# Performance work log

Hardware: AMD Instinct MI355X
Metric: run time of the kernel (lower is better)

Reference implementation:

```python
import jax, jax.numpy as jnp
import numpy as np

B, S, D = 8, 2048, 512

def setup_inputs() -> dict:
    key = jax.random.key(0)
    k1, k2 = jax.random.split(key)
    lstm_out = jax.random.normal(k1, (B, S, D), dtype=jnp.float32)
    # xavier_uniform init for [D, D]
    limit = float(np.sqrt(6.0 / (D + D)))
    attention_weights = jax.random.uniform(k2, (D, D), dtype=jnp.float32, minval=-limit, maxval=limit)
    return {"lstm_out": lstm_out, "attention_weights": attention_weights}

def reference(lstm_out, attention_weights):
    # scores[b,i,j] = tanh( (x W) x^T )
    proj = jnp.einsum('bsd,de->bse', lstm_out, attention_weights)          # [B,S,D]
    scores = jnp.tanh(jnp.einsum('bsd,btd->bst', proj, lstm_out))          # [B,S,S]
    attn = jax.nn.softmax(scores, axis=-1)                                 # [B,S,S]
    return jnp.einsum('bst,btd->bsd', attn, lstm_out)                      # [B,S,D]
```

## Files before the change

### kernel.cpp

```cpp
#include <hip/hip_runtime.h>
#include <hip/hip_bf16.h>

typedef __bf16 bf16;
typedef __attribute__((ext_vector_type(8))) __bf16 bf16x8;
typedef __attribute__((ext_vector_type(4))) float floatx4;

#define NPART 16
#define NSLOT 32

__device__ __forceinline__ void gl_lds16(const bf16* g, bf16* l) {
    __builtin_amdgcn_global_load_lds(
        (const __attribute__((address_space(1))) unsigned int*)g,
        (__attribute__((address_space(3))) unsigned int*)l,
        16, 0, 0);
}

__device__ __forceinline__ void swizzle_mn(int& bm, int& bn) {
    int gx = gridDim.x;
    int f  = blockIdx.y * gx + blockIdx.x;
    int st = f >> 3, r = f & 7;
    int mgroups = gx >> 2;
    bm = (st % mgroups) * 4 + (r & 3);
    bn = (st / mgroups) * 2 + (r >> 2);
}

__global__ __launch_bounds__(256) void cast_both(const float* __restrict__ in,
                                                 bf16* __restrict__ outn,
                                                 bf16* __restrict__ outt,
                                                 int R, int C) {
    __shared__ float tile[32][33];
    const long long bz = blockIdx.z;
    in   += bz * (long long)R * C;
    outn += bz * (long long)R * C;
    outt += bz * (long long)R * C;
    const int r0 = blockIdx.x * 32, c0 = blockIdx.y * 32;
    const int tx = threadIdx.x & 31, ty = threadIdx.x >> 5;
#pragma unroll
    for (int i = 0; i < 32; i += 8) {
        float v = in[(long long)(r0 + ty + i) * C + (c0 + tx)];
        tile[ty + i][tx] = v;
        outn[(long long)(r0 + ty + i) * C + (c0 + tx)] = (bf16)v;
    }
    __syncthreads();
#pragma unroll
    for (int i = 0; i < 32; i += 8)
        outt[(long long)(c0 + ty + i) * R + (r0 + tx)] = (bf16)tile[tx][ty + i];
}

__global__ __launch_bounds__(256) void cast_transpose(const float* __restrict__ in,
                                                      bf16* __restrict__ out,
                                                      int R, int C) {
    __shared__ float tile[32][33];
    const int r0 = blockIdx.x * 32, c0 = blockIdx.y * 32;
    const int tx = threadIdx.x & 31, ty = threadIdx.x >> 5;
#pragma unroll
    for (int i = 0; i < 32; i += 8)
        tile[ty + i][tx] = in[(long long)(r0 + ty + i) * C + (c0 + tx)];
    __syncthreads();
#pragma unroll
    for (int i = 0; i < 32; i += 8)
        out[(long long)(c0 + ty + i) * R + (r0 + tx)] = (bf16)tile[tx][ty + i];
}

__device__ __forceinline__ float fast_tanh(float v) {
    float e = __expf(2.0f * v);
    return 1.0f - 2.0f / (e + 1.0f);
}

template <int MODE>
__global__ __launch_bounds__(256) void gemm128(const bf16* __restrict__ A,
                                               const bf16* __restrict__ Bm,
                                               void* __restrict__ Cout,
                                               float* __restrict__ rpart,
                                               int M, int N, int K,
                                               long long batchA, long long batchB,
                                               long long batchC, long long batchR) {
    const long long bz = blockIdx.z;
    A  += bz * batchA;
    Bm += bz * batchB;

    __shared__ bf16 As[2][128 * 64];
    __shared__ bf16 Bs[2][128 * 64];
    __shared__ float rs[128];

    const int t    = threadIdx.x;
    const int lane = t & 63;
    const int wave = t >> 6;
    const int quad = lane >> 4;
    const int l16  = lane & 15;

    int bm, bn;
    swizzle_mn(bm, bn);
    const int m0 = bm * 128;
    const int n0 = bn * 128;
    const int wm = (wave >> 1) * 64;
    const int wn = (wave & 1) * 64;

    floatx4 acc[4][4] = {};

    const int ra = t >> 3;
    const int ca = (((t & 7) ^ (ra & 7))) * 8;
    const long long rstep = 32LL * K;
    const bf16* Abase = A + (long long)(m0 + ra) * K + ca;
    const bf16* Bbase = Bm + (long long)(n0 + ra) * K + ca;

    const int cq0 = ((quad) ^ (l16 & 7)) * 8;
    const int cq1 = ((4 + quad) ^ (l16 & 7)) * 8;

    if (MODE == 2) {
        if (t < 128) {
            const float* pp = rpart + (bz * batchR + m0 + t) * NSLOT;
            float s = 0.f;
#pragma unroll
            for (int c = 0; c < NSLOT / 4; ++c) {
                float4 p = ((const float4*)pp)[c];
                s += (p.x + p.y) + (p.z + p.w);
            }
            rs[t] = 1.0f / s;
        }
    }

    auto stage = [&](int buf, int k0) {
#pragma unroll
        for (int i = 0; i < 4; ++i) {
            gl_lds16(Abase + k0 + i * rstep, &As[buf][(t + 256 * i) * 8]);
            gl_lds16(Bbase + k0 + i * rstep, &Bs[buf][(t + 256 * i) * 8]);
        }
    };

    auto compute = [&](int buf) {
#pragma unroll
        for (int s = 0; s < 2; ++s) {
            const int cq = s ? cq1 : cq0;
            bf16x8 af[4], bfr[4];
#pragma unroll
            for (int i = 0; i < 4; ++i)
                af[i] = *(const bf16x8*)(&As[buf][(wm + i * 16 + l16) * 64 + cq]);
#pragma unroll
            for (int j = 0; j < 4; ++j)
                bfr[j] = *(const bf16x8*)(&Bs[buf][(wn + j * 16 + l16) * 64 + cq]);
#pragma unroll
            for (int i = 0; i < 4; ++i)
#pragma unroll
                for (int j = 0; j < 4; ++j)
                    acc[i][j] = __builtin_amdgcn_mfma_f32_16x16x32_bf16(af[i], bfr[j], acc[i][j], 0, 0, 0);
        }
    };

    stage(0, 0);
    __syncthreads();

    for (int k0 = 0; k0 < K; k0 += 128) {
        if (k0 + 64 < K) stage(1, k0 + 64);
        compute(0);
        __syncthreads();
        if (k0 + 128 < K) stage(0, k0 + 128);
        compute(1);
        __syncthreads();
    }

    if (MODE == 1) {
        bf16* Cg = (bf16*)Cout + bz * batchC;
        const int slot = bn * 2 + (wave & 1);
#pragma unroll
        for (int i = 0; i < 4; ++i)
#pragma unroll
            for (int r = 0; r < 4; ++r) {
                long long row = m0 + wm + i * 16 + quad * 4 + r;
                float s = 0.f;
#pragma unroll
                for (int j = 0; j < 4; ++j) {
                    float v = __expf(fast_tanh(acc[i][j][r]));
                    s += v;
                    Cg[row * (long long)N + (n0 + wn + j * 16 + l16)] = (bf16)v;
                }
#pragma unroll
                for (int msk = 1; msk < 16; msk <<= 1) s += __shfl_xor(s, msk);
                if (l16 == 0)
                    rpart[(bz * batchR + row) * NSLOT + slot] = s;
            }
    } else {
        float* Og = (float*)Cout + bz * batchC;
#pragma unroll
        for (int i = 0; i < 4; ++i)
#pragma unroll
            for (int r = 0; r < 4; ++r) {
                int rl = wm + i * 16 + quad * 4 + r;
                float inv = rs[rl];
                long long row = m0 + rl;
#pragma unroll
                for (int j = 0; j < 4; ++j)
                    Og[row * (long long)N + (n0 + wn + j * 16 + l16)] = acc[i][j][r] * inv;
            }
    }
}

__global__ __launch_bounds__(256) void gemm64_nt(const bf16* __restrict__ A,
                                                 const bf16* __restrict__ Bm,
                                                 bf16* __restrict__ Cout,
                                                 int M, int N, int K) {
    __shared__ bf16 As[2][64 * 64];
    __shared__ bf16 Bs[2][128 * 64];

    const int t    = threadIdx.x;
    const int lane = t & 63;
    const int wave = t >> 6;
    const int quad = lane >> 4;
    const int l16  = lane & 15;

    const int m0 = blockIdx.x * 64;
    const int n0 = blockIdx.y * 128;
    const int wn = wave * 32;

    floatx4 acc[4][2] = {};

    const int ra = t >> 3;
    const int ca = (((t & 7) ^ (ra & 7))) * 8;
    const long long rstep = 32LL * K;
    const bf16* Abase = A + (long long)(m0 + ra) * K + ca;
    const bf16* Bbase = Bm + (long long)(n0 + ra) * K + ca;

    const int cq0 = ((quad) ^ (l16 & 7)) * 8;
    const int cq1 = ((4 + quad) ^ (l16 & 7)) * 8;

    auto stage = [&](int buf, int k0) {
#pragma unroll
        for (int i = 0; i < 2; ++i)
            gl_lds16(Abase + k0 + i * rstep, &As[buf][(t + 256 * i) * 8]);
#pragma unroll
        for (int i = 0; i < 4; ++i)
            gl_lds16(Bbase + k0 + i * rstep, &Bs[buf][(t + 256 * i) * 8]);
    };

    auto compute = [&](int buf) {
#pragma unroll
        for (int s = 0; s < 2; ++s) {
            const int cq = s ? cq1 : cq0;
            bf16x8 af[4], bfr[2];
#pragma unroll
            for (int i = 0; i < 4; ++i)
                af[i] = *(const bf16x8*)(&As[buf][(i * 16 + l16) * 64 + cq]);
#pragma unroll
            for (int j = 0; j < 2; ++j)
                bfr[j] = *(const bf16x8*)(&Bs[buf][(wn + j * 16 + l16) * 64 + cq]);
#pragma unroll
            for (int i = 0; i < 4; ++i)
#pragma unroll
                for (int j = 0; j < 2; ++j)
                    acc[i][j] = __builtin_amdgcn_mfma_f32_16x16x32_bf16(af[i], bfr[j], acc[i][j], 0, 0, 0);
        }
    };

    stage(0, 0);
    __syncthreads();

    for (int k0 = 0; k0 < K; k0 += 128) {
        if (k0 + 64 < K) stage(1, k0 + 64);
        compute(0);
        __syncthreads();
        if (k0 + 128 < K) stage(0, k0 + 128);
        compute(1);
        __syncthreads();
    }

#pragma unroll
    for (int i = 0; i < 4; ++i)
#pragma unroll
        for (int r = 0; r < 4; ++r) {
            long long row = m0 + i * 16 + quad * 4 + r;
#pragma unroll
            for (int j = 0; j < 2; ++j)
                Cout[row * (long long)N + (n0 + wn + j * 16 + l16)] = (bf16)acc[i][j][r];
        }
}

extern "C" void kernel_launch(void* const* d_in, const int* in_sizes, int n_in,
                              void* d_out, int out_size, void* d_ws, size_t ws_size,
                              hipStream_t stream) {
    const int B = 8, S = 2048, D = 512;
    const float* x = (const float*)d_in[0];
    const float* W = (const float*)d_in[1];
    float* out = (float*)d_out;

    const size_t nx = (size_t)B * S * D;
    const size_t nw = (size_t)D * D;

    char* ws = (char*)d_ws;
    auto al = [](size_t v) { return (v + 255) & ~(size_t)255; };
    size_t off = 0;
    bf16* xb = (bf16*)(ws + off); off = al(off + nx * 2);
    bf16* xt = (bf16*)(ws + off); off = al(off + nx * 2);
    bf16* pb = (bf16*)(ws + off); off = al(off + nx * 2);
    bf16* wt = (bf16*)(ws + off); off = al(off + nw * 2);
    float* rpart = (float*)(ws + off); off = al(off + (size_t)B * S * NSLOT * 4);
    bf16* sb = (bf16*)(ws + off);
    const size_t full_need = off + (size_t)B * S * S * 2;
    const bool batched = (ws_size >= full_need);

    { dim3 g(S / 32, D / 32, B); cast_both<<<g, 256, 0, stream>>>(x, xb, xt, S, D); }
    { dim3 g(D / 32, D / 32, 1); cast_transpose<<<g, 256, 0, stream>>>(W, wt, D, D); }

    {
        dim3 g(B * S / 64, D / 128, 1);
        gemm64_nt<<<g, 256, 0, stream>>>(xb, wt, pb, B * S, D, D);
    }

    const long long sd = (long long)S * D;
    const long long ss = (long long)S * S;

    if (batched) {
        dim3 g2(S / 128, S / 128, B);
        gemm128<1><<<g2, 256, 0, stream>>>(pb, xb, (void*)sb, rpart, S, S, D, sd, sd, ss, S);
        dim3 g4(S / 128, D / 128, B);
        gemm128<2><<<g4, 256, 0, stream>>>(sb, xt, (void*)out, rpart, S, D, S, ss, sd, sd, S);
    } else {
        for (int b = 0; b < B; ++b) {
            dim3 g2(S / 128, S / 128, 1);
            gemm128<1><<<g2, 256, 0, stream>>>(pb + (size_t)b * sd, xb + (size_t)b * sd,
                                               (void*)sb, rpart + (size_t)b * S * NSLOT,
                                               S, S, D, 0, 0, 0, S);
            dim3 g4(S / 128, D / 128, 1);
            gemm128<2><<<g4, 256, 0, stream>>>(sb, xt + (size_t)b * sd,
                                               (void*)(out + (size_t)b * sd), rpart + (size_t)b * S * NSLOT,
                                               S, D, S, 0, 0, 0, S);
        }
    }
}
```

Measured before the change: 203.9 us.

## Enlarge GEMM tiles to 256x128 with 8 waves and triple-buffered async loads

Result: slower. 234.3 us (+14.9%).

```diff
diff --git a/kernel.cpp b/kernel.cpp
--- a/kernel.cpp
+++ b/kernel.cpp
@@ -68,7 +68,7 @@
 }
 
 template <int MODE>
-__global__ __launch_bounds__(256) void gemm128(const bf16* __restrict__ A,
+__global__ __launch_bounds__(512) void gemm256(const bf16* __restrict__ A,
                                                const bf16* __restrict__ Bm,
                                                void* __restrict__ Cout,
                                                float* __restrict__ rpart,
@@ -79,36 +79,33 @@
     A  += bz * batchA;
     Bm += bz * batchB;
 
-    __shared__ bf16 As[2][128 * 64];
-    __shared__ bf16 Bs[2][128 * 64];
-    __shared__ float rs[128];
+    __shared__ bf16 As[3][256 * 64];
+    __shared__ bf16 Bs[3][128 * 64];
+    __shared__ float rs[256];
 
     const int t    = threadIdx.x;
     const int lane = t & 63;
-    const int wave = t >> 6;
+    const int wid  = t >> 6;
     const int quad = lane >> 4;
     const int l16  = lane & 15;
+    const int wr   = wid >> 1;
+    const int wc   = wid & 1;
 
     int bm, bn;
     swizzle_mn(bm, bn);
-    const int m0 = bm * 128;
+    const int m0 = bm * 256;
     const int n0 = bn * 128;
-    const int wm = (wave >> 1) * 64;
-    const int wn = (wave & 1) * 64;
 
     floatx4 acc[4][4] = {};
 
-    const int ra = t >> 3;
-    const int ca = (((t & 7) ^ (ra & 7))) * 8;
-    const long long rstep = 32LL * K;
-    const bf16* Abase = A + (long long)(m0 + ra) * K + ca;
-    const bf16* Bbase = Bm + (long long)(n0 + ra) * K + ca;
-
-    const int cq0 = ((quad) ^ (l16 & 7)) * 8;
-    const int cq1 = ((4 + quad) ^ (l16 & 7)) * 8;
+    const int ra  = t >> 3;
+    const int ca8 = (((t & 7) ^ (ra & 7))) * 8;
+    const long long rstep = 64LL * K;
+    const bf16* Abase = A + (long long)(m0 + ra) * K + ca8;
+    const bf16* Bbase = Bm + (long long)(n0 + ra) * K + ca8;
 
     if (MODE == 2) {
-        if (t < 128) {
+        if (t < 256) {
             const float* pp = rpart + (bz * batchR + m0 + t) * NSLOT;
             float s = 0.f;
 #pragma unroll
@@ -120,59 +117,69 @@
         }
     }
 
-    auto stage = [&](int buf, int k0) {
-#pragma unroll
-        for (int i = 0; i < 4; ++i) {
-            gl_lds16(Abase + k0 + i * rstep, &As[buf][(t + 256 * i) * 8]);
-            gl_lds16(Bbase + k0 + i * rstep, &Bs[buf][(t + 256 * i) * 8]);
-        }
+    const int NT = K >> 6;
+
+    auto stage = [&](int buf, int kt) {
+        const long long k0 = (long long)kt * 64;
+#pragma unroll
+        for (int i = 0; i < 4; ++i)
+            gl_lds16(Abase + k0 + i * rstep, &As[buf][(t + 512 * i) * 8]);
+#pragma unroll
+        for (int i = 0; i < 2; ++i)
+            gl_lds16(Bbase + k0 + i * rstep, &Bs[buf][(t + 512 * i) * 8]);
     };
 
     auto compute = [&](int buf) {
 #pragma unroll
         for (int s = 0; s < 2; ++s) {
-            const int cq = s ? cq1 : cq0;
+            const int cq = ((s * 4 + quad) ^ (l16 & 7)) * 8;
             bf16x8 af[4], bfr[4];
 #pragma unroll
             for (int i = 0; i < 4; ++i)
-                af[i] = *(const bf16x8*)(&As[buf][(wm + i * 16 + l16) * 64 + cq]);
+                af[i] = *(const bf16x8*)(&As[buf][(wr * 64 + i * 16 + l16) * 64 + cq]);
 #pragma unroll
             for (int j = 0; j < 4; ++j)
-                bfr[j] = *(const bf16x8*)(&Bs[buf][(wn + j * 16 + l16) * 64 + cq]);
+                bfr[j] = *(const bf16x8*)(&Bs[buf][(wc * 64 + j * 16 + l16) * 64 + cq]);
+            __builtin_amdgcn_s_setprio(1);
 #pragma unroll
             for (int i = 0; i < 4; ++i)
 #pragma unroll
                 for (int j = 0; j < 4; ++j)
                     acc[i][j] = __builtin_amdgcn_mfma_f32_16x16x32_bf16(af[i], bfr[j], acc[i][j], 0, 0, 0);
+            __builtin_amdgcn_s_setprio(0);
         }
     };
 
     stage(0, 0);
-    __syncthreads();
-
-    for (int k0 = 0; k0 < K; k0 += 128) {
-        if (k0 + 64 < K) stage(1, k0 + 64);
-        compute(0);
-        __syncthreads();
-        if (k0 + 128 < K) stage(0, k0 + 128);
-        compute(1);
-        __syncthreads();
-    }
+    stage(1, 1);
+    asm volatile("s_waitcnt vmcnt(6)\n\ts_barrier" ::: "memory");
+
+    for (int kt = 0; kt < NT - 1; ++kt) {
+        if (kt + 2 < NT) {
+            stage((kt + 2) % 3, kt + 2);
+            compute(kt % 3);
+            asm volatile("s_waitcnt vmcnt(6)\n\ts_barrier" ::: "memory");
+        } else {
+            compute(kt % 3);
+            asm volatile("s_waitcnt vmcnt(0)\n\ts_barrier" ::: "memory");
+        }
+    }
+    compute((NT - 1) % 3);
 
     if (MODE == 1) {
         bf16* Cg = (bf16*)Cout + bz * batchC;
-        const int slot = bn * 2 + (wave & 1);
+        const int slot = bn * 2 + wc;
 #pragma unroll
         for (int i = 0; i < 4; ++i)
 #pragma unroll
             for (int r = 0; r < 4; ++r) {
-                long long row = m0 + wm + i * 16 + quad * 4 + r;
+                long long row = m0 + wr * 64 + i * 16 + quad * 4 + r;
                 float s = 0.f;
 #pragma unroll
                 for (int j = 0; j < 4; ++j) {
                     float v = __expf(fast_tanh(acc[i][j][r]));
                     s += v;
-                    Cg[row * (long long)N + (n0 + wn + j * 16 + l16)] = (bf16)v;
+                    Cg[row * (long long)N + (n0 + wc * 64 + j * 16 + l16)] = (bf16)v;
                 }
 #pragma unroll
                 for (int msk = 1; msk < 16; msk <<= 1) s += __shfl_xor(s, msk);
@@ -185,12 +192,12 @@
         for (int i = 0; i < 4; ++i)
 #pragma unroll
             for (int r = 0; r < 4; ++r) {
-                int rl = wm + i * 16 + quad * 4 + r;
+                int rl = wr * 64 + i * 16 + quad * 4 + r;
                 float inv = rs[rl];
                 long long row = m0 + rl;
 #pragma unroll
                 for (int j = 0; j < 4; ++j)
-                    Og[row * (long long)N + (n0 + wn + j * 16 + l16)] = acc[i][j][r] * inv;
+                    Og[row * (long long)N + (n0 + wc * 64 + j * 16 + l16)] = acc[i][j][r] * inv;
             }
     }
 }
@@ -309,18 +316,18 @@
     const long long ss = (long long)S * S;
 
     if (batched) {
-        dim3 g2(S / 128, S / 128, B);
-        gemm128<1><<<g2, 256, 0, stream>>>(pb, xb, (void*)sb, rpart, S, S, D, sd, sd, ss, S);
-        dim3 g4(S / 128, D / 128, B);
-        gemm128<2><<<g4, 256, 0, stream>>>(sb, xt, (void*)out, rpart, S, D, S, ss, sd, sd, S);
+        dim3 g2(S / 256, S / 128, B);
+        gemm256<1><<<g2, 512, 0, stream>>>(pb, xb, (void*)sb, rpart, S, S, D, sd, sd, ss, S);
+        dim3 g4(S / 256, D / 128, B);
+        gemm256<2><<<g4, 512, 0, stream>>>(sb, xt, (void*)out, rpart, S, D, S, ss, sd, sd, S);
     } else {
         for (int b = 0; b < B; ++b) {
-            dim3 g2(S / 128, S / 128, 1);
-            gemm128<1><<<g2, 256, 0, stream>>>(pb + (size_t)b * sd, xb + (size_t)b * sd,
+            dim3 g2(S / 256, S / 128, 1);
+            gemm256<1><<<g2, 512, 0, stream>>>(pb + (size_t)b * sd, xb + (size_t)b * sd,
                                                (void*)sb, rpart + (size_t)b * S * NSLOT,
                                                S, S, D, 0, 0, 0, S);
-            dim3 g4(S / 128, D / 128, 1);
-            gemm128<2><<<g4, 256, 0, stream>>>(sb, xt + (size_t)b * sd,
+            dim3 g4(S / 256, D / 128, 1);
+            gemm256<2><<<g4, 512, 0, stream>>>(sb, xt + (size_t)b * sd,
                                                (void*)(out + (size_t)b * sd), rpart + (size_t)b * S * NSLOT,
                                                S, D, S, 0, 0, 0, S);
         }
```
